# Performance work log

Hardware: AMD Instinct MI355X
Metric: run time of the kernel (lower is better)

The kernel has to match this reference:

```python
import jax, jax.numpy as jnp
import numpy as np

B, S, D_IN, D_H = 8, 2048, 512, 512

def setup_inputs() -> dict:
    key = jax.random.key(0)
    ks = jax.random.split(key, 7)
    s = 1.0 / np.sqrt(D_IN)
    return {
        "x": jax.random.normal(ks[0], (B, S, D_IN), dtype=jnp.float32),
        "Wq": jax.random.uniform(ks[1], (D_H, D_IN), jnp.float32, -s, s),
        "bq": jax.random.uniform(ks[2], (D_H,), jnp.float32, -s, s),
        "Wk": jax.random.uniform(ks[3], (D_H, D_IN), jnp.float32, -s, s),
        "bk": jax.random.uniform(ks[4], (D_H,), jnp.float32, -s, s),
        "Wv": jax.random.uniform(ks[5], (D_H, D_IN), jnp.float32, -s, s),
        "bv": jax.random.uniform(ks[6], (D_H,), jnp.float32, -s, s),
    }

def reference(x, Wq, bq, Wk, bk, Wv, bv):
    # torch Linear: y = x @ W.T + b
    Q = jnp.einsum('bsd,hd->bsh', x, Wq) + bq
    K = jnp.einsum('bsd,hd->bsh', x, Wk) + bk
    V = jnp.einsum('bsd,hd->bsh', x, Wv) + bv
    scale = jnp.sqrt(jnp.asarray(D_H, dtype=x.dtype))
    scores = jnp.einsum('bqh,bkh->bqk', Q, K) / scale  # [B,S,S]
    attn = jax.nn.softmax(scores, axis=-1)
    return jnp.einsum('bqk,bkh->bqh', attn, V)
```

## Files before the change

### kernel.cpp

```cpp
#include <hip/hip_runtime.h>
#include <hip/hip_bf16.h>
#include <cstdint>

#define B_   8
#define S_   2048
#define DIN  512
#define DH   512

typedef __attribute__((ext_vector_type(8))) short  short8;
typedef __attribute__((ext_vector_type(4))) short  short4_;
typedef __attribute__((ext_vector_type(4))) float  float4_;

__device__ inline unsigned short f2bf(float f) {
    union { float f; unsigned u; } v; v.f = f;
    unsigned u = v.u;
    u += 0x7fffu + ((u >> 16) & 1u);
    return (unsigned short)(u >> 16);
}

__device__ inline void gload_lds16(const void* g, void* l) {
    __builtin_amdgcn_global_load_lds(
        (const __attribute__((address_space(1))) void*)g,
        (__attribute__((address_space(3))) void*)l, 16, 0, 0);
}

__global__ __launch_bounds__(256) void conv_bf16(
    const float* __restrict__ x,
    const float* __restrict__ Wq, const float* __restrict__ Wk, const float* __restrict__ Wv,
    unsigned short* __restrict__ xb, unsigned short* __restrict__ wb)
{
    const int NX4 = (B_ * S_ * DIN) / 4;
    const int NW4 = (DH * DIN) / 4;
    const int total = NX4 + 3 * NW4;
    for (int i = blockIdx.x * blockDim.x + threadIdx.x; i < total;
         i += gridDim.x * blockDim.x) {
        const float4_* src; unsigned short* dst; int j;
        if (i < NX4)             { src = (const float4_*)x;  dst = xb;            j = i; }
        else if (i < NX4 + NW4)  { src = (const float4_*)Wq; dst = wb;            j = i - NX4; }
        else if (i < NX4 + 2*NW4){ src = (const float4_*)Wk; dst = wb + DH*DIN;   j = i - NX4 - NW4; }
        else                     { src = (const float4_*)Wv; dst = wb + 2*DH*DIN; j = i - NX4 - 2*NW4; }
        float4_ v = src[j];
        short4_ o;
        o[0] = (short)f2bf(v[0]); o[1] = (short)f2bf(v[1]);
        o[2] = (short)f2bf(v[2]); o[3] = (short)f2bf(v[3]);
        ((short4_*)dst)[j] = o;
    }
}

__global__ __launch_bounds__(256) void qkv_gemm(
    const unsigned short* __restrict__ xb,
    const unsigned short* __restrict__ wb,
    const float* __restrict__ bq, const float* __restrict__ bk, const float* __restrict__ bv,
    unsigned short* __restrict__ qws, unsigned short* __restrict__ kws,
    unsigned short* __restrict__ vt2)
{
    __shared__ __align__(16) unsigned short smem[17408];

    const int tm   = blockIdx.x;
    const int tc   = blockIdx.y;
    const int mat  = tc >> 2;
    const int nb   = (tc & 3) * 128;
    const int tid  = threadIdx.x;
    const int w    = tid >> 6;
    const int lane = tid & 63;
    const int l15  = lane & 15;
    const int quad = lane >> 4;
    const int wm   = (w & 1) * 64;
    const int wn   = (w >> 1) * 64;
    const int m0   = tm * 128;

    const unsigned short* wmat = wb + (size_t)mat * DH * DIN;

    float4_ zero = {0.f, 0.f, 0.f, 0.f};
    float4_ acc[4][4];
    #pragma unroll
    for (int i = 0; i < 4; i++)
        #pragma unroll
        for (int j = 0; j < 4; j++) acc[i][j] = zero;

    const int lr = lane >> 2;
    const int lb = (lane & 3) * 16;

    auto stage = [&](int kk, int bufi) {
        unsigned short* Ab = smem + bufi * 8192;
        unsigned short* Bb = smem + 4096 + bufi * 8192;
        #pragma unroll
        for (int c = 0; c < 2; c++) {
            int r = w * 32 + c * 16;
            const unsigned char* gA = (const unsigned char*)(xb + (size_t)(m0 + r) * DIN + kk);
            gload_lds16(gA + (size_t)lr * (DIN * 2) + lb, (void*)(Ab + r * 32));
            const unsigned char* gB = (const unsigned char*)(wmat + (size_t)(nb + r) * DIN + kk);
            gload_lds16(gB + (size_t)lr * (DIN * 2) + lb, (void*)(Bb + r * 32));
        }
    };

    stage(0, 0);
    for (int ki = 0; ki < 16; ki++) {
        __syncthreads();
        if (ki < 15) stage((ki + 1) * 32, (ki + 1) & 1);
        const unsigned short* Ab = smem + (ki & 1) * 8192;
        const unsigned short* Bb = smem + 4096 + (ki & 1) * 8192;
        short8 af[4], bf[4];
        #pragma unroll
        for (int mt = 0; mt < 4; mt++)
            af[mt] = *(const short8*)(Ab + (wm + mt * 16 + l15) * 32 + quad * 8);
        #pragma unroll
        for (int nt = 0; nt < 4; nt++)
            bf[nt] = *(const short8*)(Bb + (wn + nt * 16 + l15) * 32 + quad * 8);
        #pragma unroll
        for (int mt = 0; mt < 4; mt++)
            #pragma unroll
            for (int nt = 0; nt < 4; nt++)
                acc[mt][nt] = __builtin_amdgcn_mfma_f32_16x16x32_bf16(af[mt], bf[nt], acc[mt][nt], 0, 0, 0);
    }

    if (mat < 2) {
        const float* bias  = (mat == 0) ? bq : bk;
        const float  scale = (mat == 0) ? 0.044194173824159216f : 1.0f;
        unsigned short* dst = (mat == 0) ? qws : kws;
        #pragma unroll
        for (int nt = 0; nt < 4; nt++) {
            int n = nb + wn + nt * 16 + l15;
            float bv_ = bias[n];
            #pragma unroll
            for (int mt = 0; mt < 4; mt++) {
                #pragma unroll
                for (int r = 0; r < 4; r++) {
                    int m = m0 + wm + mt * 16 + quad * 4 + r;
                    dst[(size_t)m * DH + n] = f2bf((acc[mt][nt][r] + bv_) * scale);
                }
            }
        }
    } else {
        __syncthreads();
        unsigned short* trans = smem;
        #pragma unroll
        for (int nt = 0; nt < 4; nt++) {
            int dloc = wn + nt * 16 + l15;
            float bv_ = bv[nb + dloc];
            #pragma unroll
            for (int mt = 0; mt < 4; mt++) {
                short4_ pk;
                #pragma unroll
                for (int r = 0; r < 4; r++) pk[r] = (short)f2bf(acc[mt][nt][r] + bv_);
                *(short4_*)(trans + dloc * 136 + wm + mt * 16 + quad * 4) = pk;
            }
        }
        __syncthreads();
        int dl   = tid >> 1;
        int h    = tid & 1;
        int dh_g = nb + dl;
        int s4   = (dh_g >> 2) & 3;
        int bi   = m0 >> 11;
        int tile0 = (m0 & 2047) >> 4;
        unsigned char* vt2b = (unsigned char*)vt2;
        #pragma unroll
        for (int t = 0; t < 4; t++) {
            int tl = h * 4 + t;
            const uint2* c = (const uint2*)(trans + dl * 136 + tl * 16);
            uint2 d0 = c[0 ^ s4], d1 = c[1 ^ s4], d2 = c[2 ^ s4], d3 = c[3 ^ s4];
            unsigned char* dst = vt2b + ((size_t)(bi * 128 + tile0 + tl) << 14) + dh_g * 32;
            ((uint2*)dst)[0] = d0; ((uint2*)dst)[1] = d1;
            ((uint2*)dst)[2] = d2; ((uint2*)dst)[3] = d3;
        }
    }
}

__global__ __launch_bounds__(512, 2) void attn(
    const unsigned short* __restrict__ qws,
    const unsigned short* __restrict__ kws,
    const unsigned short* __restrict__ vt2,
    float* __restrict__ out)
{
    __shared__ __align__(16) unsigned char smem[141824];

    const int bid  = blockIdx.x;
    const int b    = bid & 7;
    const int qt_b = bid >> 3;
    const int tid  = threadIdx.x;
    const int w    = tid >> 6;
    const int g    = w >> 2;
    const int wl   = w & 3;
    const int lane = tid & 63;
    const int l15  = lane & 15;
    const int quad = lane >> 4;

    const int qrow0  = b * S_ + qt_b * 64;
    const int myqrow = qrow0 + wl * 16;

    const unsigned short* kgrp = kws + (size_t)(b * S_ + g * 1024) * DH;
    const unsigned char*  vtb  = (const unsigned char*)vt2;

    unsigned char* kb    = smem + g * 65536;
    unsigned char* vb    = smem + g * 65536 + 32768;
    unsigned char* pbase = smem + 131072 + g * 5120;
    float*         lbuf  = (float*)(smem + 141312);

    short8 qf[16];
    {
        const short8* qp = (const short8*)(qws + (size_t)(myqrow + l15) * DH);
        #pragma unroll
        for (int ksi = 0; ksi < 16; ksi++) qf[ksi] = qp[ksi * 4 + quad];
    }

    float4_ zero = {0.f, 0.f, 0.f, 0.f};
    float4_ o[32];
    #pragma unroll
    for (int i = 0; i < 32; i++) o[i] = zero;
    float4_ ol[4];
    #pragma unroll
    for (int i = 0; i < 4; i++) ol[i] = zero;

    short4_ ones;
    ones[0] = ones[1] = ones[2] = ones[3] = (short)0x3F80;

    auto stageK = [&](int n, int bufi) {
        #pragma unroll
        for (int i = 0; i < 4; i++) {
            int row = wl * 4 + i;
            const unsigned char* gp =
                (const unsigned char*)(kgrp + (size_t)(n * 16 + row) * DH);
            gload_lds16(gp + ((lane ^ (row & 7)) << 4),
                        kb + bufi * 16384 + row * 1024);
        }
    };
    auto stageV = [&](int n, int bufi) {
        const unsigned char* base =
            vtb + ((size_t)(b * 128 + g * 64 + n) << 14) + wl * 4096;
        #pragma unroll
        for (int i = 0; i < 4; i++)
            gload_lds16(base + i * 1024 + lane * 16,
                        vb + bufi * 16384 + wl * 4096 + i * 1024);
    };

    auto doPV = [&](int bufi) {
        const unsigned char* vt_ = vb + bufi * 16384;
        const unsigned char* pp  = pbase + bufi * 2560;
        short4_ pa[4];
        #pragma unroll
        for (int qt = 0; qt < 4; qt++)
            pa[qt] = *(const short4_*)(pp + (qt * 16 + l15) * 40 + quad * 8);
        #pragma unroll
        for (int qt = 0; qt < 4; qt++)
            ol[qt] = __builtin_amdgcn_mfma_f32_16x16x16bf16_1k(pa[qt], ones, ol[qt], 0, 0, 0);
        #pragma unroll
        for (int dht = 0; dht < 8; dht++) {
            int dh_sl = wl * 128 + dht * 16 + l15;
            short4_ vf = *(const short4_*)(vt_ + dh_sl * 32 + ((quad ^ ((dh_sl >> 2) & 3)) << 3));
            #pragma unroll
            for (int qt = 0; qt < 4; qt++)
                o[qt * 8 + dht] = __builtin_amdgcn_mfma_f32_16x16x16bf16_1k(pa[qt], vf, o[qt * 8 + dht], 0, 0, 0);
        }
    };

    stageK(0, 0);

    for (int it = 0; it < 64; it++) {
        __syncthreads();

        if (it < 63) stageK(it + 1, (it + 1) & 1);
        stageV(it, it & 1);

        const unsigned char* kt_ = kb + (it & 1) * 16384;
        float4_ s0 = zero, s1 = zero;
        #pragma unroll
        for (int ksi = 0; ksi < 16; ksi += 2) {
            short8 k0 = *(const short8*)(kt_ + l15 * 1024 + ((( ksi      * 4 + quad) ^ (l15 & 7)) << 4));
            short8 k1 = *(const short8*)(kt_ + l15 * 1024 + ((((ksi + 1) * 4 + quad) ^ (l15 & 7)) << 4));
            s0 = __builtin_amdgcn_mfma_f32_16x16x32_bf16(qf[ksi],     k0, s0, 0, 0, 0);
            s1 = __builtin_amdgcn_mfma_f32_16x16x32_bf16(qf[ksi + 1], k1, s1, 0, 0, 0);
        }
        float4_ sc = s0 + s1;

        unsigned short* pp = (unsigned short*)(pbase + (it & 1) * 2560);
        #pragma unroll
        for (int r = 0; r < 4; r++)
            pp[(wl * 16 + quad * 4 + r) * 20 + l15] = f2bf(__expf(sc[r]));

        if (it) doPV((it - 1) & 1);
    }

    __syncthreads();
    doPV(1);

    if (wl == 0 && l15 == 0) {
        #pragma unroll
        for (int qt = 0; qt < 4; qt++)
            #pragma unroll
            for (int r = 0; r < 4; r++)
                lbuf[g * 64 + qt * 16 + quad * 4 + r] = ol[qt][r];
    }
    __syncthreads();
    if (g == 1) {
        float* om = (float*)(smem + wl * 33280);
        #pragma unroll
        for (int qt = 0; qt < 4; qt++)
            #pragma unroll
            for (int dht = 0; dht < 8; dht++)
                #pragma unroll
                for (int r = 0; r < 4; r++)
                    om[(qt * 16 + quad * 4 + r) * 130 + dht * 16 + l15] = o[qt * 8 + dht][r];
    }
    __syncthreads();
    if (g == 0) {
        const float* om = (const float*)(smem + wl * 33280);
        #pragma unroll
        for (int qt = 0; qt < 4; qt++) {
            float rl[4];
            #pragma unroll
            for (int r = 0; r < 4; r++) {
                int row = qt * 16 + quad * 4 + r;
                rl[r] = 1.f / (lbuf[row] + lbuf[64 + row]);
            }
            #pragma unroll
            for (int dht = 0; dht < 8; dht++)
                #pragma unroll
                for (int r = 0; r < 4; r++) {
                    int row = qt * 16 + quad * 4 + r;
                    out[(size_t)(qrow0 + row) * DH + wl * 128 + dht * 16 + l15] =
                        (o[qt * 8 + dht][r] + om[row * 130 + dht * 16 + l15]) * rl[r];
                }
        }
    }
}

extern "C" void kernel_launch(void* const* d_in, const int* in_sizes, int n_in,
                              void* d_out, int out_size, void* d_ws, size_t ws_size,
                              hipStream_t stream) {
    const float* x  = (const float*)d_in[0];
    const float* Wq = (const float*)d_in[1];
    const float* bq = (const float*)d_in[2];
    const float* Wk = (const float*)d_in[3];
    const float* bk = (const float*)d_in[4];
    const float* Wv = (const float*)d_in[5];
    const float* bv = (const float*)d_in[6];
    float* out = (float*)d_out;

    unsigned short* qws = (unsigned short*)d_ws;
    unsigned short* kws = qws + (size_t)B_ * S_ * DH;
    unsigned short* vt2 = kws + (size_t)B_ * S_ * DH;

    unsigned short* xb = (unsigned short*)d_out;
    unsigned short* wb = xb + (size_t)B_ * S_ * DIN;

    conv_bf16<<<dim3(2048), dim3(256), 0, stream>>>(x, Wq, Wk, Wv, xb, wb);
    qkv_gemm<<<dim3(128, 12), dim3(256), 0, stream>>>(xb, wb, bq, bk, bv, qws, kws, vt2);
    attn<<<dim3(256), dim3(512), 0, stream>>>(qws, kws, vt2, out);
}
```

Before: 279.9 us.

## Load V fragments directly to registers, shrink LDS, accumulate row sums in VALU

V tiles are now read straight from global memory into registers each iteration instead of being staged through LDS, which roughly halves the shared-memory footprint and may allow more blocks per CU. The row-sum MFMA against a ones vector is replaced by per-lane accumulation plus a DPP cross-lane reduction, and exp is switched to exp2 with log2(e) folded into the Q scale. The V layout store drops the swizzle and uses 16-byte writes, and s_setprio wraps the MFMA sections. Cross-group output reduction is split into two passes so it fits in the smaller LDS, at the cost of extra barriers and exposed global-load latency for V.

Result: slower. 289.2 us (+3.3%).

```diff
diff --git a/kernel.cpp b/kernel.cpp
--- a/kernel.cpp
+++ b/kernel.cpp
@@ -22,6 +22,18 @@
     __builtin_amdgcn_global_load_lds(
         (const __attribute__((address_space(1))) void*)g,
         (__attribute__((address_space(3))) void*)l, 16, 0, 0);
+}
+
+template <int C>
+__device__ inline float fdpp(float x) {
+    return __int_as_float(__builtin_amdgcn_update_dpp(0, __float_as_int(x), C, 0xF, 0xF, true));
+}
+__device__ inline float rsum16(float v) {
+    v += fdpp<0x140>(v);
+    v += fdpp<0x141>(v);
+    v += fdpp<27>(v);
+    v += fdpp<177>(v);
+    return v;
 }
 
 __global__ __launch_bounds__(256) void conv_bf16(
@@ -116,7 +128,7 @@
 
     if (mat < 2) {
         const float* bias  = (mat == 0) ? bq : bk;
-        const float  scale = (mat == 0) ? 0.044194173824159216f : 1.0f;
+        const float  scale = (mat == 0) ? 0.06375870430742225f : 1.0f;
         unsigned short* dst = (mat == 0) ? qws : kws;
         #pragma unroll
         for (int nt = 0; nt < 4; nt++) {
@@ -150,18 +162,16 @@
         int dl   = tid >> 1;
         int h    = tid & 1;
         int dh_g = nb + dl;
-        int s4   = (dh_g >> 2) & 3;
         int bi   = m0 >> 11;
         int tile0 = (m0 & 2047) >> 4;
         unsigned char* vt2b = (unsigned char*)vt2;
         #pragma unroll
         for (int t = 0; t < 4; t++) {
             int tl = h * 4 + t;
-            const uint2* c = (const uint2*)(trans + dl * 136 + tl * 16);
-            uint2 d0 = c[0 ^ s4], d1 = c[1 ^ s4], d2 = c[2 ^ s4], d3 = c[3 ^ s4];
+            const uint4* c = (const uint4*)(trans + dl * 136 + tl * 16);
             unsigned char* dst = vt2b + ((size_t)(bi * 128 + tile0 + tl) << 14) + dh_g * 32;
-            ((uint2*)dst)[0] = d0; ((uint2*)dst)[1] = d1;
-            ((uint2*)dst)[2] = d2; ((uint2*)dst)[3] = d3;
+            ((uint4*)dst)[0] = c[0];
+            ((uint4*)dst)[1] = c[1];
         }
     }
 }
@@ -172,7 +182,7 @@
     const unsigned short* __restrict__ vt2,
     float* __restrict__ out)
 {
-    __shared__ __align__(16) unsigned char smem[141824];
+    __shared__ __align__(16) unsigned char smem[76288];
 
     const int bid  = blockIdx.x;
     const int b    = bid & 7;
@@ -191,10 +201,9 @@
     const unsigned short* kgrp = kws + (size_t)(b * S_ + g * 1024) * DH;
     const unsigned char*  vtb  = (const unsigned char*)vt2;
 
-    unsigned char* kb    = smem + g * 65536;
-    unsigned char* vb    = smem + g * 65536 + 32768;
-    unsigned char* pbase = smem + 131072 + g * 5120;
-    float*         lbuf  = (float*)(smem + 141312);
+    unsigned char* kb    = smem + g * 32768;
+    unsigned char* pbase = smem + 65536 + g * 5120;
+    float*         lbuf  = (float*)(smem + 75776);
 
     short8 qf[16];
     {
@@ -207,12 +216,9 @@
     float4_ o[32];
     #pragma unroll
     for (int i = 0; i < 32; i++) o[i] = zero;
-    float4_ ol[4];
-    #pragma unroll
-    for (int i = 0; i < 4; i++) ol[i] = zero;
-
-    short4_ ones;
-    ones[0] = ones[1] = ones[2] = ones[3] = (short)0x3F80;
+    float l_[4] = {0.f, 0.f, 0.f, 0.f};
+
+    short4_ vreg[8];
 
     auto stageK = [&](int n, int bufi) {
         #pragma unroll
@@ -224,33 +230,28 @@
                         kb + bufi * 16384 + row * 1024);
         }
     };
-    auto stageV = [&](int n, int bufi) {
-        const unsigned char* base =
-            vtb + ((size_t)(b * 128 + g * 64 + n) << 14) + wl * 4096;
-        #pragma unroll
-        for (int i = 0; i < 4; i++)
-            gload_lds16(base + i * 1024 + lane * 16,
-                        vb + bufi * 16384 + wl * 4096 + i * 1024);
+
+    auto loadV = [&](int n) {
+        const unsigned char* base = vtb + ((size_t)(b * 128 + g * 64 + n) << 14)
+                                  + (size_t)(wl * 128 + l15) * 32 + quad * 8;
+        #pragma unroll
+        for (int dht = 0; dht < 8; dht++)
+            vreg[dht] = *(const short4_*)(base + dht * 512);
     };
 
     auto doPV = [&](int bufi) {
-        const unsigned char* vt_ = vb + bufi * 16384;
-        const unsigned char* pp  = pbase + bufi * 2560;
+        const unsigned char* pp = pbase + bufi * 2560;
         short4_ pa[4];
         #pragma unroll
         for (int qt = 0; qt < 4; qt++)
             pa[qt] = *(const short4_*)(pp + (qt * 16 + l15) * 40 + quad * 8);
-        #pragma unroll
-        for (int qt = 0; qt < 4; qt++)
-            ol[qt] = __builtin_amdgcn_mfma_f32_16x16x16bf16_1k(pa[qt], ones, ol[qt], 0, 0, 0);
-        #pragma unroll
-        for (int dht = 0; dht < 8; dht++) {
-            int dh_sl = wl * 128 + dht * 16 + l15;
-            short4_ vf = *(const short4_*)(vt_ + dh_sl * 32 + ((quad ^ ((dh_sl >> 2) & 3)) << 3));
+        __builtin_amdgcn_s_setprio(1);
+        #pragma unroll
+        for (int dht = 0; dht < 8; dht++)
             #pragma unroll
             for (int qt = 0; qt < 4; qt++)
-                o[qt * 8 + dht] = __builtin_amdgcn_mfma_f32_16x16x16bf16_1k(pa[qt], vf, o[qt * 8 + dht], 0, 0, 0);
-        }
+                o[qt * 8 + dht] = __builtin_amdgcn_mfma_f32_16x16x16bf16_1k(pa[qt], vreg[dht], o[qt * 8 + dht], 0, 0, 0);
+        __builtin_amdgcn_s_setprio(0);
     };
 
     stageK(0, 0);
@@ -258,11 +259,12 @@
     for (int it = 0; it < 64; it++) {
         __syncthreads();
 
+        if (it) loadV(it - 1);
         if (it < 63) stageK(it + 1, (it + 1) & 1);
-        stageV(it, it & 1);
 
         const unsigned char* kt_ = kb + (it & 1) * 16384;
         float4_ s0 = zero, s1 = zero;
+        __builtin_amdgcn_s_setprio(1);
         #pragma unroll
         for (int ksi = 0; ksi < 16; ksi += 2) {
             short8 k0 = *(const short8*)(kt_ + l15 * 1024 + ((( ksi      * 4 + quad) ^ (l15 & 7)) << 4));
@@ -270,56 +272,65 @@
             s0 = __builtin_amdgcn_mfma_f32_16x16x32_bf16(qf[ksi],     k0, s0, 0, 0, 0);
             s1 = __builtin_amdgcn_mfma_f32_16x16x32_bf16(qf[ksi + 1], k1, s1, 0, 0, 0);
         }
+        __builtin_amdgcn_s_setprio(0);
         float4_ sc = s0 + s1;
 
         unsigned short* pp = (unsigned short*)(pbase + (it & 1) * 2560);
         #pragma unroll
+        for (int r = 0; r < 4; r++) {
+            float p = __builtin_exp2f(sc[r]);
+            l_[r] += p;
+            pp[(wl * 16 + quad * 4 + r) * 20 + l15] = f2bf(p);
+        }
+
+        if (it) doPV((it - 1) & 1);
+    }
+
+    __syncthreads();
+    loadV(63);
+    doPV(1);
+
+    float lsum[4];
+    #pragma unroll
+    for (int r = 0; r < 4; r++) lsum[r] = rsum16(l_[r]);
+    if (l15 == 0) {
+        #pragma unroll
         for (int r = 0; r < 4; r++)
-            pp[(wl * 16 + quad * 4 + r) * 20 + l15] = f2bf(__expf(sc[r]));
-
-        if (it) doPV((it - 1) & 1);
-    }
-
-    __syncthreads();
-    doPV(1);
-
-    if (wl == 0 && l15 == 0) {
-        #pragma unroll
-        for (int qt = 0; qt < 4; qt++)
-            #pragma unroll
-            for (int r = 0; r < 4; r++)
-                lbuf[g * 64 + qt * 16 + quad * 4 + r] = ol[qt][r];
-    }
-    __syncthreads();
-    if (g == 1) {
-        float* om = (float*)(smem + wl * 33280);
-        #pragma unroll
-        for (int qt = 0; qt < 4; qt++)
-            #pragma unroll
-            for (int dht = 0; dht < 8; dht++)
-                #pragma unroll
-                for (int r = 0; r < 4; r++)
-                    om[(qt * 16 + quad * 4 + r) * 130 + dht * 16 + l15] = o[qt * 8 + dht][r];
-    }
-    __syncthreads();
-    if (g == 0) {
-        const float* om = (const float*)(smem + wl * 33280);
-        #pragma unroll
-        for (int qt = 0; qt < 4; qt++) {
-            float rl[4];
-            #pragma unroll
-            for (int r = 0; r < 4; r++) {
-                int row = qt * 16 + quad * 4 + r;
-                rl[r] = 1.f / (lbuf[row] + lbuf[64 + row]);
-            }
-            #pragma unroll
-            for (int dht = 0; dht < 8; dht++)
+            lbuf[g * 64 + wl * 16 + quad * 4 + r] = lsum[r];
+    }
+
+    float* om = (float*)(smem + (wl & 1) * 33280);
+    #pragma unroll
+    for (int p = 0; p < 2; p++) {
+        __syncthreads();
+        if (g == 1 && (wl >> 1) == p) {
+            #pragma unroll
+            for (int qt = 0; qt < 4; qt++)
+                #pragma unroll
+                for (int dht = 0; dht < 8; dht++)
+                    #pragma unroll
+                    for (int r = 0; r < 4; r++)
+                        om[(qt * 16 + quad * 4 + r) * 130 + dht * 16 + l15] = o[qt * 8 + dht][r];
+        }
+        __syncthreads();
+        if (g == 0 && (wl >> 1) == p) {
+            #pragma unroll
+            for (int qt = 0; qt < 4; qt++) {
+                float rl[4];
                 #pragma unroll
                 for (int r = 0; r < 4; r++) {
                     int row = qt * 16 + quad * 4 + r;
-                    out[(size_t)(qrow0 + row) * DH + wl * 128 + dht * 16 + l15] =
-                        (o[qt * 8 + dht][r] + om[row * 130 + dht * 16 + l15]) * rl[r];
+                    rl[r] = 1.f / (lbuf[row] + lbuf[64 + row]);
                 }
+                #pragma unroll
+                for (int dht = 0; dht < 8; dht++)
+                    #pragma unroll
+                    for (int r = 0; r < 4; r++) {
+                        int row = qt * 16 + quad * 4 + r;
+                        out[(size_t)(qrow0 + row) * DH + wl * 128 + dht * 16 + l15] =
+                            (o[qt * 8 + dht][r] + om[row * 130 + dht * 16 + l15]) * rl[r];
+                    }
+            }
         }
     }
 }
```
